# Kernel tuning notes

Measured on AMD Instinct MI355X. Metric: run time of the kernel, lower is better.

Reference implementation:

```python
import jax, jax.numpy as jnp
import numpy as np

B, S, D = 8, 1024, 1024
H, DK = 16, 64  # heads, key_size (== head_size)
NEG = 1e12


def setup_inputs() -> dict:
    key = jax.random.key(0)
    ks = jax.random.split(key, 10)
    s = 1.0 / np.sqrt(D)
    return {
        "q": jax.random.normal(ks[0], (B, S, D), jnp.float32),
        "k": jax.random.normal(ks[1], (B, S, D), jnp.float32),
        "v": jax.random.normal(ks[2], (B, S, D), jnp.float32),
        "pos_bias": jax.random.normal(ks[3], (S, S, DK), jnp.float32) * 0.02,
        "Wq": jax.random.normal(ks[4], (D, H * DK), jnp.float32) * s,
        "Wk": jax.random.normal(ks[5], (D, H * DK), jnp.float32) * s,
        "Wv": jax.random.normal(ks[6], (D, H * DK), jnp.float32) * s,
        "Wo": jax.random.normal(ks[7], (H * DK, D), jnp.float32) * s,
        "bq": jnp.zeros((H * DK,), jnp.float32),
        "bk": jnp.zeros((H * DK,), jnp.float32),
        "bv": jnp.zeros((H * DK,), jnp.float32),
        "bo": jnp.zeros((D,), jnp.float32),
        "q_mask": jnp.ones((B, S), jnp.int32),
        "v_mask": jnp.ones((B, S), jnp.int32),
    }


def reference(q, k, v, pos_bias, Wq, Wk, Wv, Wo, bq, bk, bv, bo, q_mask, v_mask):
    qm = q_mask.astype(q.dtype)  # [B,Sq]
    vm = v_mask.astype(q.dtype)  # [B,Sk]
    # Projections (faithful quirk: K is projected from v, as in the source)
    qw = (q @ Wq + bq).reshape(B, S, H, DK)
    kw = (v @ Wk + bk).reshape(B, S, H, DK)
    vw = (v @ Wv + bv).reshape(B, S, H, DK)
    # scores + inline relative-position bias ('typial_relative' branch)
    a = jnp.einsum('bjhd,bkhd->bhjk', qw, kw)
    a = a + jnp.einsum('bjhd,jkd->bhjk', qw, pos_bias)
    a = a / jnp.sqrt(jnp.asarray(DK, a.dtype))
    # additive key mask, then softmax over keys
    a = a - (1.0 - vm)[:, None, None, :] * NEG
    a = jax.nn.softmax(a, axis=-1)
    o = jnp.einsum('bhjk,bkhd->bjhd', a, vw)  # [B,Sq,H,DK]
    o = o.reshape(B, S, H * DK) @ Wo + bo
    # multiplicative query mask on output
    o = o * qm[:, :, None]
    return o
```

## Files before the change

kernel.cpp:

```cpp
#include <hip/hip_runtime.h>

using short8 = __attribute__((ext_vector_type(8))) short;
using f32x4  = __attribute__((ext_vector_type(4))) float;
using u16x4  = __attribute__((ext_vector_type(4))) unsigned short;
using fl4    = __attribute__((ext_vector_type(4))) float;

#define MFMA16(a, b, c) __builtin_amdgcn_mfma_f32_16x16x32_bf16((a), (b), (c), 0, 0, 0)

static __device__ __forceinline__ unsigned short f2bf(float f) {
  union { float f; unsigned u; } x; x.f = f;
  return (unsigned short)((x.u + 0x7FFFu + ((x.u >> 16) & 1u)) >> 16);
}
static __device__ __forceinline__ float bf2f(unsigned short s) {
  union { unsigned u; float f; } x; x.u = ((unsigned)s) << 16;
  return x.f;
}
static __device__ __forceinline__ float fexp2(float x) {
  float r; asm("v_exp_f32 %0, %1" : "=v"(r) : "v"(x)); return r;
}
static __device__ __forceinline__ unsigned pk2(float lo, float hi) {
  unsigned r; asm("v_cvt_pk_bf16_f32 %0, %1, %2" : "=v"(r) : "v"(lo), "v"(hi));
  return r;
}

static __device__ __forceinline__ void gload16(const void* g, void* l) {
  __builtin_amdgcn_global_load_lds((const __attribute__((address_space(1))) void*)g,
                                   (__attribute__((address_space(3))) void*)l, 16, 0, 0);
}

#define LOG2E 1.4426950408889634f

__global__ __launch_bounds__(256) void k_wconv4(
    const float* __restrict__ W0, const float* __restrict__ W1,
    const float* __restrict__ W2, const float* __restrict__ W3,
    unsigned short* __restrict__ Wt0, unsigned short* __restrict__ Wt1,
    unsigned short* __restrict__ Wt2, unsigned short* __restrict__ Wt3) {
  const float* W = (blockIdx.z == 0) ? W0 : (blockIdx.z == 1) ? W1
                   : (blockIdx.z == 2) ? W2 : W3;
  unsigned short* Wt = (blockIdx.z == 0) ? Wt0 : (blockIdx.z == 1) ? Wt1
                       : (blockIdx.z == 2) ? Wt2 : Wt3;
  __shared__ float tile[64][65];
  const int t = threadIdx.x;
  const int n0 = blockIdx.x * 64, k0 = blockIdx.y * 64;
#pragma unroll
  for (int p = 0; p < 4; ++p) {
    int row = p * 16 + (t >> 4);
    int c4 = (t & 15) * 4;
    fl4 val = *(const fl4*)&W[(size_t)(k0 + row) * 1024 + n0 + c4];
    tile[row][c4 + 0] = val[0];
    tile[row][c4 + 1] = val[1];
    tile[row][c4 + 2] = val[2];
    tile[row][c4 + 3] = val[3];
  }
  __syncthreads();
#pragma unroll
  for (int p = 0; p < 4; ++p) {
    int n = p * 16 + (t >> 4);
    int k4 = (t & 15) * 4;
    u16x4 u;
    u[0] = f2bf(tile[k4 + 0][n]);
    u[1] = f2bf(tile[k4 + 1][n]);
    u[2] = f2bf(tile[k4 + 2][n]);
    u[3] = f2bf(tile[k4 + 3][n]);
    *(u16x4*)&Wt[(size_t)(n0 + n) * 1024 + k0 + k4] = u;
  }
}

__global__ __launch_bounds__(256) void k_cvt(const float* __restrict__ a,
                                             const float* __restrict__ b,
                                             unsigned short* __restrict__ oa,
                                             unsigned short* __restrict__ ob) {
  const float* src = blockIdx.y ? b : a;
  unsigned short* dst = blockIdx.y ? ob : oa;
  size_t i = ((size_t)blockIdx.x * 256 + threadIdx.x) * 8;
  fl4 v0 = *(const fl4*)&src[i];
  fl4 v1 = *(const fl4*)&src[i + 4];
  u16x4 u0, u1;
  u0[0] = f2bf(v0[0]); u0[1] = f2bf(v0[1]); u0[2] = f2bf(v0[2]); u0[3] = f2bf(v0[3]);
  u1[0] = f2bf(v1[0]); u1[1] = f2bf(v1[1]); u1[2] = f2bf(v1[2]); u1[3] = f2bf(v1[3]);
  *(u16x4*)&dst[i] = u0;
  *(u16x4*)&dst[i + 4] = u1;
}

#define GEMM3_CORE(APTR, BPTR)                                                  \
  const int t = threadIdx.x, lane = t & 63, w = t >> 6;                         \
  const int g = lane >> 4, ln = lane & 15;                                      \
  const int wm = w >> 1, wn = w & 1;                                            \
  __shared__ unsigned short sh[24576];    \
  const int srow = lane >> 2;                                                   \
  const int sc = (lane & 3) ^ ((lane >> 3) & 3);                                \
  const int rsw = ((ln >> 1) & 3);                                              \
  f32x4 acc[4][4] = {};                                                         \
  _Pragma("unroll") for (int pre = 0; pre < 2; ++pre) {                         \
    _Pragma("unroll") for (int p = 0; p < 2; ++p) {                             \
      gload16(&APTR[(size_t)(m0 + p * 64 + w * 16 + srow) * 1024 + pre * 32 + sc * 8], \
              &sh[pre * 8192 + (p * 64 + w * 16) * 32]);                        \
      gload16(&BPTR[(size_t)(n0 + p * 64 + w * 16 + srow) * 1024 + pre * 32 + sc * 8], \
              &sh[pre * 8192 + 4096 + (p * 64 + w * 16) * 32]);                 \
    }                                                                           \
  }                                                                             \
  int cur = 0;                                                                  \
  for (int tt = 0; tt < 32; ++tt) {                                             \
    if (tt < 31) {                                                              \
      asm volatile("s_waitcnt vmcnt(4)" ::: "memory");                          \
    } else {                                                                    \
      asm volatile("s_waitcnt vmcnt(0)" ::: "memory");                          \
    }                                                                           \
    __builtin_amdgcn_sched_barrier(0);                                          \
    __builtin_amdgcn_s_barrier();                                               \
    __builtin_amdgcn_sched_barrier(0);                                          \
    if (tt < 30) {                                                              \
      int bb = cur + 2; if (bb >= 3) bb -= 3;                                   \
      int kk = (tt + 2) * 32;                                                   \
      _Pragma("unroll") for (int p = 0; p < 2; ++p) {                           \
        gload16(&APTR[(size_t)(m0 + p * 64 + w * 16 + srow) * 1024 + kk + sc * 8], \
                &sh[bb * 8192 + (p * 64 + w * 16) * 32]);                       \
        gload16(&BPTR[(size_t)(n0 + p * 64 + w * 16 + srow) * 1024 + kk + sc * 8], \
                &sh[bb * 8192 + 4096 + (p * 64 + w * 16) * 32]);                \
      }                                                                         \
    }                                                                           \
    const unsigned short* As = &sh[cur * 8192];                                 \
    const unsigned short* Bs = As + 4096;                                       \
    short8 af[4], bfr[4];                                                       \
    _Pragma("unroll") for (int fm = 0; fm < 4; ++fm)                            \
        af[fm] = *(const short8*)&As[(wm * 64 + fm * 16 + ln) * 32 + (g ^ rsw) * 8]; \
    _Pragma("unroll") for (int fn = 0; fn < 4; ++fn)                            \
        bfr[fn] = *(const short8*)&Bs[(wn * 64 + fn * 16 + ln) * 32 + (g ^ rsw) * 8]; \
    _Pragma("unroll") for (int fn = 0; fn < 4; ++fn) {                          \
      _Pragma("unroll") for (int fm = 0; fm < 4; ++fm)                          \
          acc[fm][fn] = MFMA16(af[fm], bfr[fn], acc[fm][fn]);                   \
    }                                                                           \
    cur = (cur == 2) ? 0 : cur + 1;                                             \
  }

__global__ __launch_bounds__(256) void k_proj3(
    const unsigned short* __restrict__ QB, const unsigned short* __restrict__ VB,
    const unsigned short* __restrict__ WtQ, const unsigned short* __restrict__ WtK,
    const unsigned short* __restrict__ WtV,
    const float* __restrict__ bq, const float* __restrict__ bk,
    const float* __restrict__ bv,
    unsigned short* __restrict__ QW, unsigned short* __restrict__ KW,
    unsigned short* __restrict__ VWT) {
  const int mode = blockIdx.z;
  const unsigned short* A8 = (mode == 0) ? QB : VB;
  const unsigned short* Wt = (mode == 0) ? WtQ : (mode == 1) ? WtK : WtV;
  const float* bias = (mode == 0) ? bq : (mode == 1) ? bk : bv;
  const int n0 = blockIdx.x * 128, m0 = blockIdx.y * 128;
  GEMM3_CORE(A8, Wt)
  __syncthreads();
  const float scale = (mode == 0) ? (0.125f * LOG2E) : 1.0f;
#pragma unroll
  for (int fn = 0; fn < 4; ++fn) {
    float bn = bias[n0 + wn * 64 + fn * 16 + ln];
#pragma unroll
    for (int fm = 0; fm < 4; ++fm) {
#pragma unroll
      for (int r = 0; r < 4; ++r) {
        float val = (acc[fm][fn][r] + bn) * scale;
        sh[(wm * 64 + fm * 16 + 4 * g + r) * 132 + wn * 64 + fn * 16 + ln] = f2bf(val);
      }
    }
  }
  __syncthreads();
  if (mode < 2) {
    unsigned short* OUT = (mode == 0) ? QW : KW;
#pragma unroll
    for (int p = 0; p < 16; ++p) {
      int row = p * 8 + (t >> 5), c4 = (t & 31) * 4;
      *(u16x4*)&OUT[(size_t)(m0 + row) * 1024 + n0 + c4] =
          *(const u16x4*)&sh[row * 132 + c4];
    }
  } else {
    const int b = m0 >> 10, s0 = m0 & 1023;
#pragma unroll
    for (int p = 0; p < 16; ++p) {
#pragma unroll
      for (int qh = 0; qh < 2; ++qh) {
        int hdl = p * 8 + (t >> 5);
        int sl = qh * 64 + (t & 31) * 2;
        unsigned lo = sh[sl * 132 + hdl];
        unsigned hi = sh[(sl + 1) * 132 + hdl];
        int hd = n0 + hdl;
        int h = hd >> 6, d = hd & 63;
        *(unsigned*)&VWT[((size_t)(b * 16 + h) * 64 + d) * 1024 + s0 + sl] =
            lo | (hi << 16);
      }
    }
  }
}

__global__ __launch_bounds__(256) void k_out3(
    const unsigned short* __restrict__ OB, const unsigned short* __restrict__ WtO,
    const float* __restrict__ bo, const int* __restrict__ qmask,
    float* __restrict__ out) {
  const int n0 = blockIdx.x * 128, m0 = blockIdx.y * 128;
  GEMM3_CORE(OB, WtO)
  float bn[4];
#pragma unroll
  for (int fn = 0; fn < 4; ++fn) bn[fn] = bo[n0 + wn * 64 + fn * 16 + ln];
#pragma unroll
  for (int fm = 0; fm < 4; ++fm) {
#pragma unroll
    for (int r = 0; r < 4; ++r) {
      int row = m0 + wm * 64 + fm * 16 + 4 * g + r;
      float qm = (float)qmask[row];
#pragma unroll
      for (int fn = 0; fn < 4; ++fn)
        out[(size_t)row * 1024 + n0 + wn * 64 + fn * 16 + ln] =
            (acc[fm][fn][r] + bn[fn]) * qm;
    }
  }
}

__global__ __launch_bounds__(256) void k_pbias(
    const unsigned short* __restrict__ QW, const float* __restrict__ pb,
    const int* __restrict__ vmask, unsigned short* __restrict__ CB, int jbase) {
  const int kt = blockIdx.x;
  const int jl = blockIdx.y;
  const int j = jbase + jl;
  const int t = threadIdx.x, lane = t & 63, w = t >> 6;
  const int g = lane >> 4, ln = lane & 15;
  const int wm = w >> 1, wn = w & 1;
  __shared__ unsigned short sm[18432];
  unsigned short* a_lds = sm;
  unsigned short* b_lds = sm + 9216;
#pragma unroll
  for (int p = 0; p < 8; ++p) {
    int i4 = p * 256 + t;
    int row = i4 >> 4, c4 = (i4 & 15) * 4;
    *(u16x4*)&a_lds[row * 72 + c4] =
        *(const u16x4*)&QW[((size_t)(row >> 4) * 1024 + j) * 1024 + (row & 15) * 64 + c4];
  }
#pragma unroll
  for (int p = 0; p < 8; ++p) {
    int i4 = p * 256 + t;
    int row = i4 >> 4, c4 = (i4 & 15) * 4;
    fl4 val = *(const fl4*)&pb[((size_t)j * 1024 + kt * 128 + row) * 64 + c4];
    u16x4 u;
    u[0] = f2bf(val[0]); u[1] = f2bf(val[1]);
    u[2] = f2bf(val[2]); u[3] = f2bf(val[3]);
    *(u16x4*)&b_lds[row * 72 + c4] = u;
  }
  __syncthreads();
  f32x4 acc[4][4] = {};
#pragma unroll
  for (int ks = 0; ks < 2; ++ks) {
    short8 af[4];
#pragma unroll
    for (int fm = 0; fm < 4; ++fm)
      af[fm] = *(const short8*)&a_lds[(wm * 64 + fm * 16 + ln) * 72 + ks * 32 + 8 * g];
#pragma unroll
    for (int fn = 0; fn < 4; ++fn) {
      short8 bfr = *(const short8*)&b_lds[(wn * 64 + fn * 16 + ln) * 72 + ks * 32 + 8 * g];
#pragma unroll
      for (int fm = 0; fm < 4; ++fm) acc[fm][fn] = MFMA16(af[fm], bfr, acc[fm][fn]);
    }
  }
  __syncthreads();
#pragma unroll
  for (int fn = 0; fn < 4; ++fn) {
    int kcol = kt * 128 + wn * 64 + fn * 16 + ln;
#pragma unroll
    for (int fm = 0; fm < 4; ++fm) {
      float off = vmask[(wm * 4 + fm) * 1024 + kcol] ? 0.f : (-1e12f * LOG2E);
#pragma unroll
      for (int r = 0; r < 4; ++r)
        sm[(wm * 64 + fm * 16 + 4 * g + r) * 132 + wn * 64 + fn * 16 + ln] =
            f2bf(acc[fm][fn][r] + off);
    }
  }
  __syncthreads();
#pragma unroll
  for (int p = 0; p < 16; ++p) {
    int row = p * 8 + (t >> 5), c4 = (t & 31) * 4;
    *(u16x4*)&CB[((size_t)row * 512 + jl) * 1024 + kt * 128 + c4] =
        *(const u16x4*)&sm[row * 132 + c4];
  }
}

__global__ __launch_bounds__(256) void k_attn(
    const unsigned short* __restrict__ QW, const unsigned short* __restrict__ KW,
    const unsigned short* __restrict__ VWT, const unsigned short* __restrict__ CB,
    unsigned short* __restrict__ OB, int jbase) {
  const int jt = blockIdx.x, h = blockIdx.y, b = blockIdx.z;
  const int t = threadIdx.x, lane = t & 63, w = t >> 6;
  const int g = lane >> 4, ln = lane & 15;
  const int j0 = jbase + jt * 64;
  const int jl0 = jt * 64;
  __shared__ unsigned short lds_k[128 * 72];
  __shared__ unsigned short lds_vt[64 * 136];
  __shared__ unsigned short lds_p[4 * 16 * 136];
  unsigned short* pw = &lds_p[w * (16 * 136)];
  short8 qf[2];
  {
    const size_t qrow = ((size_t)b * 1024 + (j0 + w * 16 + ln)) * 1024 + h * 64;
    qf[0] = *(const short8*)&QW[qrow + 8 * g];
    qf[1] = *(const short8*)&QW[qrow + 32 + 8 * g];
  }
  const size_t cb_row = ((size_t)(b * 16 + h) * 512 + jl0 + w * 16 + ln) * 1024;

  u16x4 rk[8], rv[8], rcb[8];
#define LOAD_KV(kt_)                                                              \
  {                                                                               \
    _Pragma("unroll") for (int p = 0; p < 8; ++p) {                               \
      int i4 = p * 256 + t;                                                       \
      int row = i4 >> 4, c4 = (i4 & 15) * 4;                                      \
      rk[p] = *(const u16x4*)&KW[((size_t)b * 1024 + (kt_) * 128 + row) * 1024 +  \
                                 h * 64 + c4];                                    \
    }                                                                             \
    _Pragma("unroll") for (int p = 0; p < 8; ++p) {                               \
      int i4 = p * 256 + t;                                                       \
      int row = i4 >> 5, c4 = (i4 & 31) * 4;                                      \
      rv[p] = *(const u16x4*)&VWT[(((size_t)b * 16 + h) * 64 + row) * 1024 +      \
                                  (kt_) * 128 + c4];                              \
    }                                                                             \
    _Pragma("unroll") for (int p = 0; p < 8; ++p)                                 \
        rcb[p] = *(const u16x4*)&CB[cb_row + (kt_) * 128 + p * 16 + 4 * g];       \
  }

  LOAD_KV(0);
  f32x4 o_acc[4] = {};
  float l_par = 0.f;

  for (int kt = 0; kt < 8; ++kt) {
    __syncthreads();
#pragma unroll
    for (int p = 0; p < 8; ++p) {
      int i4 = p * 256 + t;
      int row = i4 >> 4, c4 = (i4 & 15) * 4;
      *(u16x4*)&lds_k[row * 72 + c4] = rk[p];
    }
#pragma unroll
    for (int p = 0; p < 8; ++p) {
      int i4 = p * 256 + t;
      int row = i4 >> 5, c4 = (i4 & 31) * 4;
      *(u16x4*)&lds_vt[row * 136 + c4] = rv[p];
    }
    f32x4 s[8];
#pragma unroll
    for (int fm = 0; fm < 8; ++fm) {
#pragma unroll
      for (int r = 0; r < 4; ++r) s[fm][r] = bf2f(rcb[fm][r]);
    }
    if (kt < 7) LOAD_KV(kt + 1);
    __syncthreads();
#pragma unroll
    for (int ks = 0; ks < 2; ++ks) {
#pragma unroll
      for (int fm = 0; fm < 8; ++fm) {
        short8 af = *(const short8*)&lds_k[(fm * 16 + ln) * 72 + ks * 32 + 8 * g];
        s[fm] = MFMA16(af, qf[ks], s[fm]);
      }
    }
#pragma unroll
    for (int fm = 0; fm < 8; ++fm) {
      float pv0 = fexp2(s[fm][0] - 17.0f);
      float pv1 = fexp2(s[fm][1] - 17.0f);
      float pv2 = fexp2(s[fm][2] - 17.0f);
      float pv3 = fexp2(s[fm][3] - 17.0f);
      l_par += (pv0 + pv1) + (pv2 + pv3);
      union { u16x4 v; unsigned u[2]; } pp;
      pp.u[0] = pk2(pv0, pv1);
      pp.u[1] = pk2(pv2, pv3);
      *(u16x4*)&pw[ln * 136 + fm * 16 + 4 * g] = pp.v;
    }
    asm volatile("s_waitcnt lgkmcnt(0)" ::: "memory");
#pragma unroll
    for (int ks = 0; ks < 4; ++ks) {
      short8 bp = *(const short8*)&pw[ln * 136 + ks * 32 + 8 * g];
#pragma unroll
      for (int fm = 0; fm < 4; ++fm) {
        short8 av = *(const short8*)&lds_vt[(fm * 16 + ln) * 136 + ks * 32 + 8 * g];
        o_acc[fm] = MFMA16(av, bp, o_acc[fm]);
      }
    }
  }
  l_par += __shfl_xor(l_par, 16);
  l_par += __shfl_xor(l_par, 32);
  float inv = 1.0f / l_par;
  const size_t orow = ((size_t)b * 1024 + (j0 + w * 16 + ln)) * 1024 + h * 64;
#pragma unroll
  for (int fm = 0; fm < 4; ++fm) {
    union { u16x4 v; unsigned u[2]; } uo;
    uo.u[0] = pk2(o_acc[fm][0] * inv, o_acc[fm][1] * inv);
    uo.u[1] = pk2(o_acc[fm][2] * inv, o_acc[fm][3] * inv);
    *(u16x4*)&OB[orow + fm * 16 + 4 * g] = uo.v;
  }
#undef LOAD_KV
}

extern "C" void kernel_launch(void* const* d_in, const int* in_sizes, int n_in,
                              void* d_out, int out_size, void* d_ws, size_t ws_size,
                              hipStream_t stream) {
  const float* q  = (const float*)d_in[0];
  const float* v  = (const float*)d_in[2];
  const float* pb = (const float*)d_in[3];
  const float* Wq = (const float*)d_in[4];
  const float* Wk = (const float*)d_in[5];
  const float* Wv = (const float*)d_in[6];
  const float* Wo = (const float*)d_in[7];
  const float* bq = (const float*)d_in[8];
  const float* bk = (const float*)d_in[9];
  const float* bv = (const float*)d_in[10];
  const float* bo = (const float*)d_in[11];
  const int* qm = (const int*)d_in[12];
  const int* vm = (const int*)d_in[13];
  float* out = (float*)d_out;

  unsigned short* ws = (unsigned short*)d_ws;
  const size_t M1 = 1024 * 1024;
  unsigned short* WTQ = ws;
  unsigned short* WTK = WTQ + M1;
  unsigned short* WTV = WTK + M1;
  unsigned short* WTO = WTV + M1;
  unsigned short* QB  = WTO + M1;
  unsigned short* VB  = QB + 8 * M1;
  unsigned short* QW  = VB + 8 * M1;
  unsigned short* KW  = QW + 8 * M1;
  unsigned short* VWT = KW + 8 * M1;
  unsigned short* OB  = VWT + 8 * M1;
  unsigned short* CB  = OB + 8 * M1;

  k_wconv4<<<dim3(16, 16, 4), 256, 0, stream>>>(Wq, Wk, Wv, Wo, WTQ, WTK, WTV, WTO);
  k_cvt<<<dim3(4096, 2), 256, 0, stream>>>(q, v, QB, VB);
  k_proj3<<<dim3(8, 64, 3), 256, 0, stream>>>(QB, VB, WTQ, WTK, WTV, bq, bk, bv,
                                              QW, KW, VWT);
  for (int st = 0; st < 2; ++st) {
    k_pbias<<<dim3(8, 512), 256, 0, stream>>>(QW, pb, vm, CB, st * 512);
    k_attn<<<dim3(8, 16, 8), 256, 0, stream>>>(QW, KW, VWT, CB, OB, st * 512);
  }
  k_out3<<<dim3(8, 64), 256, 0, stream>>>(OB, WTO, bo, qm, out);
}
```

Baseline: 386.4 us.

## Read K and V fragments directly from global memory in attention kernel

```diff
diff --git a/kernel.cpp b/kernel.cpp
--- a/kernel.cpp
+++ b/kernel.cpp
@@ -278,7 +278,7 @@
   }
 }
 
-__global__ __launch_bounds__(256) void k_attn(
+__global__ __launch_bounds__(256, 4) void k_attn(
     const unsigned short* __restrict__ QW, const unsigned short* __restrict__ KW,
     const unsigned short* __restrict__ VWT, const unsigned short* __restrict__ CB,
     unsigned short* __restrict__ OB, int jbase) {
@@ -287,8 +287,6 @@
   const int g = lane >> 4, ln = lane & 15;
   const int j0 = jbase + jt * 64;
   const int jl0 = jt * 64;
-  __shared__ unsigned short lds_k[128 * 72];
-  __shared__ unsigned short lds_vt[64 * 136];
   __shared__ unsigned short lds_p[4 * 16 * 136];
   unsigned short* pw = &lds_p[w * (16 * 136)];
   short8 qf[2];
@@ -298,57 +296,26 @@
     qf[1] = *(const short8*)&QW[qrow + 32 + 8 * g];
   }
   const size_t cb_row = ((size_t)(b * 16 + h) * 512 + jl0 + w * 16 + ln) * 1024;
-
-  u16x4 rk[8], rv[8], rcb[8];
-#define LOAD_KV(kt_)                                                              \
-  {                                                                               \
-    _Pragma("unroll") for (int p = 0; p < 8; ++p) {                               \
-      int i4 = p * 256 + t;                                                       \
-      int row = i4 >> 4, c4 = (i4 & 15) * 4;                                      \
-      rk[p] = *(const u16x4*)&KW[((size_t)b * 1024 + (kt_) * 128 + row) * 1024 +  \
-                                 h * 64 + c4];                                    \
-    }                                                                             \
-    _Pragma("unroll") for (int p = 0; p < 8; ++p) {                               \
-      int i4 = p * 256 + t;                                                       \
-      int row = i4 >> 5, c4 = (i4 & 31) * 4;                                      \
-      rv[p] = *(const u16x4*)&VWT[(((size_t)b * 16 + h) * 64 + row) * 1024 +      \
-                                  (kt_) * 128 + c4];                              \
-    }                                                                             \
-    _Pragma("unroll") for (int p = 0; p < 8; ++p)                                 \
-        rcb[p] = *(const u16x4*)&CB[cb_row + (kt_) * 128 + p * 16 + 4 * g];       \
-  }
-
-  LOAD_KV(0);
+  const unsigned short* Kb = &KW[(size_t)b * 1024 * 1024 + h * 64];
+  const unsigned short* Vb = &VWT[((size_t)(b * 16 + h) * 64) * 1024];
+
   f32x4 o_acc[4] = {};
   float l_par = 0.f;
 
   for (int kt = 0; kt < 8; ++kt) {
-    __syncthreads();
-#pragma unroll
-    for (int p = 0; p < 8; ++p) {
-      int i4 = p * 256 + t;
-      int row = i4 >> 4, c4 = (i4 & 15) * 4;
-      *(u16x4*)&lds_k[row * 72 + c4] = rk[p];
-    }
-#pragma unroll
-    for (int p = 0; p < 8; ++p) {
-      int i4 = p * 256 + t;
-      int row = i4 >> 5, c4 = (i4 & 31) * 4;
-      *(u16x4*)&lds_vt[row * 136 + c4] = rv[p];
-    }
     f32x4 s[8];
 #pragma unroll
     for (int fm = 0; fm < 8; ++fm) {
-#pragma unroll
-      for (int r = 0; r < 4; ++r) s[fm][r] = bf2f(rcb[fm][r]);
-    }
-    if (kt < 7) LOAD_KV(kt + 1);
-    __syncthreads();
+      u16x4 c = *(const u16x4*)&CB[cb_row + kt * 128 + fm * 16 + 4 * g];
+#pragma unroll
+      for (int r = 0; r < 4; ++r) s[fm][r] = bf2f(c[r]);
+    }
 #pragma unroll
     for (int ks = 0; ks < 2; ++ks) {
 #pragma unroll
       for (int fm = 0; fm < 8; ++fm) {
-        short8 af = *(const short8*)&lds_k[(fm * 16 + ln) * 72 + ks * 32 + 8 * g];
+        short8 af = *(const short8*)&Kb[(size_t)(kt * 128 + fm * 16 + ln) * 1024 +
+                                        ks * 32 + 8 * g];
         s[fm] = MFMA16(af, qf[ks], s[fm]);
       }
     }
@@ -365,12 +332,14 @@
       *(u16x4*)&pw[ln * 136 + fm * 16 + 4 * g] = pp.v;
     }
     asm volatile("s_waitcnt lgkmcnt(0)" ::: "memory");
+    __builtin_amdgcn_sched_barrier(0);
 #pragma unroll
     for (int ks = 0; ks < 4; ++ks) {
       short8 bp = *(const short8*)&pw[ln * 136 + ks * 32 + 8 * g];
 #pragma unroll
       for (int fm = 0; fm < 4; ++fm) {
-        short8 av = *(const short8*)&lds_vt[(fm * 16 + ln) * 136 + ks * 32 + 8 * g];
+        short8 av = *(const short8*)&Vb[(size_t)(fm * 16 + ln) * 1024 +
+                                        kt * 128 + ks * 32 + 8 * g];
         o_acc[fm] = MFMA16(av, bp, o_acc[fm]);
       }
     }
@@ -386,7 +355,6 @@
     uo.u[1] = pk2(o_acc[fm][2] * inv, o_acc[fm][3] * inv);
     *(u16x4*)&OB[orow + fm * 16 + 4 * g] = uo.v;
   }
-#undef LOAD_KV
 }
 
 extern "C" void kernel_launch(void* const* d_in, const int* in_sizes, int n_in,
```

New measurement: 539.4 us. 1.4x slower.
